# Performance work log

Measured on AMD Instinct MI355X. Metric: run time of the kernel, lower is better.

Reference implementation:

```python
import jax, jax.numpy as jnp
import numpy as np

B, L, H, O = 2048, 256, 512, 1  # batch, input_len, hidden_size, output_size
EPS = 1e-5

def setup_inputs() -> dict:
    key = jax.random.key(0)
    ks = jax.random.split(key, 16)
    s = 0.05
    return {
        "x": jax.random.normal(ks[0], (B, 1, O), jnp.float32),
        "hidden": jax.random.normal(ks[1], (1, B, H), jnp.float32),
        "encoder_outputs": jax.random.normal(ks[2], (B, L, H), jnp.float32),
        # weights stored [in, out] (transposed torch Linear convention)
        "emb_W": jax.random.normal(ks[3], (O, H), jnp.float32) * s,
        "emb_b": jax.random.normal(ks[4], (H,), jnp.float32) * s,
        "attn_W": jax.random.normal(ks[5], (2 * H, L), jnp.float32) * s,
        "attn_b": jax.random.normal(ks[6], (L,), jnp.float32) * s,
        "comb_W": jax.random.normal(ks[7], (2 * H, H), jnp.float32) * s,
        "comb_b": jax.random.normal(ks[8], (H,), jnp.float32) * s,
        "gru_Wih": jax.random.normal(ks[9], (H, 3 * H), jnp.float32) * s,
        "gru_Whh": jax.random.normal(ks[10], (H, 3 * H), jnp.float32) * s,
        "gru_bih": jax.random.normal(ks[11], (3 * H,), jnp.float32) * s,
        "gru_bhh": jax.random.normal(ks[12], (3 * H,), jnp.float32) * s,
        "out_W": jax.random.normal(ks[13], (H, O), jnp.float32) * s,
        "out_b": jax.random.normal(ks[14], (O,), jnp.float32) * s,
    }

def reference(x, hidden, encoder_outputs, emb_W, emb_b, attn_W, attn_b,
              comb_W, comb_b, gru_Wih, gru_Whh, gru_bih, gru_bhh, out_W, out_b):
    # embedding + InstanceNorm1d over hidden dim (C=1 channel, length=H), no affine
    embedded = x @ emb_W + emb_b                      # [B,1,H]
    mu = jnp.mean(embedded, axis=-1, keepdims=True)
    var = jnp.var(embedded, axis=-1, keepdims=True)   # biased var, matches torch
    embedded = (embedded - mu) * jax.lax.rsqrt(var + EPS)
    # dropout = identity (inference)
    h_b = jnp.transpose(hidden, (1, 0, 2))            # [B,1,H]
    attn_logits = jnp.concatenate([embedded, h_b], axis=2) @ attn_W + attn_b  # [B,1,L]
    attn_weights = jax.nn.softmax(attn_logits, axis=2)
    attn_applied = jnp.einsum('bql,bld->bqd', attn_weights, encoder_outputs)  # [B,1,H]
    out = jnp.concatenate([embedded, attn_applied], axis=2) @ comb_W + comb_b
    out = jax.nn.relu(out)                            # [B,1,H]
    # single GRU step (num_layers=1, seq_len=1)
    xt = out[:, 0, :]                                 # [B,H]
    h0 = hidden[0]                                    # [B,H]
    gi = xt @ gru_Wih + gru_bih                       # [B,3H]
    gh = h0 @ gru_Whh + gru_bhh
    i_r, i_z, i_n = jnp.split(gi, 3, axis=-1)
    h_r, h_z, h_n = jnp.split(gh, 3, axis=-1)
    r = jax.nn.sigmoid(i_r + h_r)
    z = jax.nn.sigmoid(i_z + h_z)
    n = jnp.tanh(i_n + r * h_n)
    h_new = (1.0 - z) * n + z * h0                    # [B,H]
    output = h_new[:, None, :] @ out_W + out_b        # [B,1,O]
    return output, h_new[None, :, :], attn_weights
```

## Files before the change

### kernel.cpp

```cpp
#include <hip/hip_runtime.h>
#include <math.h>

#define NB 2048
#define NL 256
#define NH 512

typedef unsigned short ushort_t;
typedef short s16x8 __attribute__((ext_vector_type(8)));
typedef short s16x4 __attribute__((ext_vector_type(4)));
typedef float f32x4 __attribute__((ext_vector_type(4)));

__device__ __forceinline__ float wsum(float v){
  #pragma unroll
  for (int o = 32; o; o >>= 1) v += __shfl_xor(v, o);
  return v;
}
__device__ __forceinline__ float wmax(float v){
  #pragma unroll
  for (int o = 32; o; o >>= 1) v = fmaxf(v, __shfl_xor(v, o));
  return v;
}
__device__ __forceinline__ ushort_t f2bf(float f){
  union { float f; unsigned u; } v; v.f = f;
  unsigned r = v.u + 0x7fffu + ((v.u >> 16) & 1u);
  return (ushort_t)(r >> 16);
}

__global__ __launch_bounds__(256)
void kPrepAll(const float* __restrict__ hidden,
              const float* __restrict__ eW, const float* __restrict__ eb,
              const float* __restrict__ attn_W, const float* __restrict__ comb_W,
              const float* __restrict__ Wih, const float* __restrict__ Whh,
              const float* __restrict__ out_b,
              ushort_t* __restrict__ A2, ushort_t* __restrict__ WTG,
              ushort_t* __restrict__ WTA, ushort_t* __restrict__ WTC,
              float* __restrict__ stats,
              float* __restrict__ p, float* __restrict__ q,
              float* __restrict__ p2, float* __restrict__ q2,
              float* __restrict__ out0)
{
  const int bid = blockIdx.x, tid = threadIdx.x;
  if (bid < 512) {
    const int idx = (bid*256 + tid) * 8;
    const int b = idx >> 9, h = idx & 511;
    float4 v0 = *(const float4*)(hidden + idx);
    float4 v1 = *(const float4*)(hidden + idx + 4);
    s16x8 o;
    o[0]=f2bf(v0.x); o[1]=f2bf(v0.y); o[2]=f2bf(v0.z); o[3]=f2bf(v0.w);
    o[4]=f2bf(v1.x); o[5]=f2bf(v1.y); o[6]=f2bf(v1.z); o[7]=f2bf(v1.w);
    *(s16x8*)&A2[(size_t)b*1024 + 512 + h] = o;
    return;
  }
  if (bid < 1024) {
    const int b2 = bid - 512, bx = b2 & 31, by = b2 >> 5;
    const int n = bx*64 + (tid & 63);
    const int ksub = by*64 + (tid >> 6)*16;
    const int g = n >> 6, t = (n >> 4) & 3, c = (g << 4) | (n & 15);
    const int sc = (t == 0) ? c : (t == 1) ? (512 + c) : (1024 + c);
    ushort_t vals[16];
    #pragma unroll
    for (int kk = 0; kk < 16; ++kk) {
      int k = ksub + kk;
      float v;
      if (k < 512) v = (t == 3) ? 0.f : Wih[(size_t)k*1536 + sc];
      else         v = (t == 2) ? 0.f : Whh[(size_t)(k-512)*1536 + sc];
      vals[kk] = f2bf(v);
    }
    *(s16x8*)&WTG[(size_t)n*1024 + ksub]     = *(s16x8*)&vals[0];
    *(s16x8*)&WTG[(size_t)n*1024 + ksub + 8] = *(s16x8*)&vals[8];
    return;
  }
  if (bid < 1056) {
    const int b2 = bid - 1024, bx = b2 & 3, by = b2 >> 2;
    const int c = bx*64 + (tid & 63);
    const int ksub = by*64 + (tid >> 6)*16;
    ushort_t vals[16];
    #pragma unroll
    for (int kk = 0; kk < 16; ++kk)
      vals[kk] = f2bf(attn_W[(size_t)(512 + ksub + kk)*NL + c]);
    *(s16x8*)&WTA[(size_t)c*512 + ksub]     = *(s16x8*)&vals[0];
    *(s16x8*)&WTA[(size_t)c*512 + ksub + 8] = *(s16x8*)&vals[8];
    return;
  }
  if (bid < 1120) {
    const int b2 = bid - 1056, bx = b2 & 7, by = b2 >> 3;
    const int c = bx*64 + (tid & 63);
    const int ksub = by*64 + (tid >> 6)*16;
    ushort_t vals[16];
    #pragma unroll
    for (int kk = 0; kk < 16; ++kk)
      vals[kk] = f2bf(comb_W[(size_t)(512 + ksub + kk)*NH + c]);
    *(s16x8*)&WTC[(size_t)c*512 + ksub]     = *(s16x8*)&vals[0];
    *(s16x8*)&WTC[(size_t)c*512 + ksub + 8] = *(s16x8*)&vals[8];
    return;
  }
  if (bid > 1132) {
    out0[(bid-1133)*256 + tid] = out_b[0];
    return;
  }
  {
    __shared__ float rw[4], rb[4];
    __shared__ float pa[4][64], pb[4][64];
    const int lane = tid & 63, wv = tid >> 6;
    float swv = eW[tid] + eW[tid + 256];
    float sbv = eb[tid] + eb[tid + 256];
    swv = wsum(swv); sbv = wsum(sbv);
    if (lane == 0) { rw[wv] = swv; rb[wv] = sbv; }
    __syncthreads();
    const float mW = (rw[0]+rw[1]+rw[2]+rw[3]) * (1.f/NH);
    const float mb = (rb[0]+rb[1]+rb[2]+rb[3]) * (1.f/NH);

    if (bid == 1132) {
      float u0 = eW[tid]-mW, u1 = eW[tid+256]-mW;
      float v0 = eb[tid]-mb, v1 = eb[tid+256]-mb;
      float s2 = u0*u0 + u1*u1, s3 = u0*v0 + u1*v1, s4 = v0*v0 + v1*v1;
      s2 = wsum(s2); s3 = wsum(s3); s4 = wsum(s4);
      if (lane == 0) { pa[0][wv] = s2; pa[1][wv] = s3; pa[2][wv] = s4; }
      __syncthreads();
      if (tid == 0) {
        stats[0] = mW; stats[1] = mb;
        stats[2] = pa[0][0]+pa[0][1]+pa[0][2]+pa[0][3];
        stats[3] = pa[1][0]+pa[1][1]+pa[1][2]+pa[1][3];
        stats[4] = pa[2][0]+pa[2][1]+pa[2][2]+pa[2][3];
      }
      return;
    }
    const int bid2 = bid - 1120;
    const float* Wsrc; int ldw, c0; float *op, *oq;
    if (bid2 < 4) { Wsrc = attn_W; ldw = NL; c0 = bid2*64;     op = p  + c0; oq = q  + c0; }
    else          { Wsrc = comb_W; ldw = NH; c0 = (bid2-4)*64; op = p2 + c0; oq = q2 + c0; }
    const int c = c0 + lane;
    const int hc = tid >> 6;
    float ap = 0.f, aq = 0.f;
    #pragma unroll 4
    for (int h = hc*128; h < hc*128 + 128; ++h) {
      float w = Wsrc[(size_t)h*ldw + c];
      ap = fmaf(eW[h]-mW, w, ap);
      aq = fmaf(eb[h]-mb, w, aq);
    }
    pa[hc][lane] = ap; pb[hc][lane] = aq;
    __syncthreads();
    if (hc == 0) {
      op[lane] = pa[0][lane]+pa[1][lane]+pa[2][lane]+pa[3][lane];
      oq[lane] = pb[0][lane]+pb[1][lane]+pb[2][lane]+pb[3][lane];
    }
  }
}

template<int EPI>
__global__ __launch_bounds__(256)
void gemm_bf16(const ushort_t* __restrict__ A, int lda,
               const ushort_t* __restrict__ Bt, int K,
               const float* __restrict__ xin, const float* __restrict__ stats,
               const float* __restrict__ pvec, const float* __restrict__ qvec,
               const float* __restrict__ bias,
               float* __restrict__ out_f, ushort_t* __restrict__ out_bf,
               const float* __restrict__ bih, const float* __restrict__ bhh,
               const float* __restrict__ hidden, const float* __restrict__ out_W,
               float* __restrict__ h_out, float* __restrict__ out0)
{
  __shared__ ushort_t As[128][72];
  __shared__ ushort_t Bs[64][72];
  const int tid = threadIdx.x, lane = tid & 63, wr = tid >> 6;
  const int m0 = blockIdx.x * 128, n0 = blockIdx.y * 64;

  f32x4 acc[2][4];
  #pragma unroll
  for (int i = 0; i < 2; ++i)
    #pragma unroll
    for (int j = 0; j < 4; ++j)
      acc[i][j] = (f32x4){0.f,0.f,0.f,0.f};

  const int srow = tid >> 3, scol = (tid & 7) * 8;
  for (int kt = 0; kt < K; kt += 64) {
    __syncthreads();
    #pragma unroll
    for (int it = 0; it < 4; ++it) {
      const int r = srow + it*32;
      *(s16x8*)&As[r][scol] = *(const s16x8*)&A[(size_t)(m0+r)*lda + kt + scol];
    }
    #pragma unroll
    for (int it = 0; it < 2; ++it) {
      const int r = srow + it*32;
      *(s16x8*)&Bs[r][scol] = *(const s16x8*)&Bt[(size_t)(n0+r)*K + kt + scol];
    }
    __syncthreads();
    #pragma unroll
    for (int ks = 0; ks < 2; ++ks) {
      const int ko = ks*32 + (lane >> 4)*8;
      s16x8 af[2], bfr[4];
      #pragma unroll
      for (int i = 0; i < 2; ++i) af[i]  = *(const s16x8*)&As[wr*32 + i*16 + (lane & 15)][ko];
      #pragma unroll
      for (int j = 0; j < 4; ++j) bfr[j] = *(const s16x8*)&Bs[j*16 + (lane & 15)][ko];
      #pragma unroll
      for (int i = 0; i < 2; ++i)
        #pragma unroll
        for (int j = 0; j < 4; ++j)
          acc[i][j] = __builtin_amdgcn_mfma_f32_16x16x32_bf16(af[i], bfr[j], acc[i][j], 0, 0, 0);
    }
  }

  if constexpr (EPI == 1 || EPI == 2) {
    const float S2 = stats[2], S3 = stats[3], S4 = stats[4];
    #pragma unroll
    for (int i = 0; i < 2; ++i) {
      #pragma unroll
      for (int reg = 0; reg < 4; ++reg) {
        const int row = m0 + wr*32 + i*16 + ((lane >> 4) << 2) + reg;
        const float xv = xin[row];
        const float rs = rsqrtf((xv*xv*S2 + 2.f*xv*S3 + S4)*(1.0f/NH) + 1e-5f);
        const float al = xv*rs, be = rs;
        #pragma unroll
        for (int j = 0; j < 4; ++j) {
          const int col = n0 + j*16 + (lane & 15);
          float v = acc[i][j][reg] + bias[col] + al*pvec[col] + be*qvec[col];
          if constexpr (EPI == 1) out_f[(size_t)row*NL + col] = v;
          else                    out_bf[(size_t)row*1024 + col] = f2bf(fmaxf(v, 0.f));
        }
      }
    }
  } else {
    const int g = n0 >> 6;
    const int hcol = (g << 4) | (lane & 15);
    const float b_r = bih[hcol]        + bhh[hcol];
    const float b_z = bih[512 + hcol]  + bhh[512 + hcol];
    const float b_i = bih[1024 + hcol];
    const float b_h = bhh[1024 + hcol];
    const float ow  = out_W[hcol];
    #pragma unroll
    for (int i = 0; i < 2; ++i) {
      #pragma unroll
      for (int reg = 0; reg < 4; ++reg) {
        const int row = m0 + wr*32 + i*16 + ((lane >> 4) << 2) + reg;
        float rv = 1.f / (1.f + expf(-(acc[i][0][reg] + b_r)));
        float zv = 1.f / (1.f + expf(-(acc[i][1][reg] + b_z)));
        float nv = tanhf(acc[i][2][reg] + b_i + rv * (acc[i][3][reg] + b_h));
        float h0v = hidden[(size_t)row*NH + hcol];
        float hn = nv + zv * (h0v - nv);
        h_out[(size_t)row*NH + hcol] = hn;
        float partial = hn * ow;
        #pragma unroll
        for (int o = 1; o < 16; o <<= 1) partial += __shfl_xor(partial, o);
        if ((lane & 15) == 0) atomicAdd(&out0[row], partial);
      }
    }
  }
}

__global__ __launch_bounds__(256)
void kStream(const float* __restrict__ logits, const float* __restrict__ enc,
             float* __restrict__ attn_out, ushort_t* __restrict__ ABF)
{
  __shared__ float wl[NL];
  __shared__ __align__(16) float4 ps[128];
  __shared__ float sred[4];
  const int tid = threadIdx.x, lane = tid & 63, wv = tid >> 6;
  const int b = blockIdx.x;

  float lg = logits[(size_t)b*NL + tid];
  float m = wmax(lg);
  if (lane == 0) sred[wv] = m;
  __syncthreads();
  m = fmaxf(fmaxf(sred[0], sred[1]), fmaxf(sred[2], sred[3]));
  float e = expf(lg - m);
  float s = wsum(e);
  __syncthreads();
  if (lane == 0) sred[wv] = s;
  __syncthreads();
  const float inv = 1.f / (sred[0] + sred[1] + sred[2] + sred[3]);
  e *= inv;
  wl[tid] = e;
  attn_out[(size_t)b*NL + tid] = e;
  __syncthreads();

  const int col = tid & 127, half = tid >> 7;
  const float4* ep = (const float4*)(enc + (size_t)b*NL*NH);
  float4 acc = {0.f,0.f,0.f,0.f};
  #pragma unroll 4
  for (int l = half*128; l < half*128 + 128; ++l) {
    float w = wl[l];
    float4 ev = ep[l*(NH/4) + col];
    acc.x = fmaf(w,ev.x,acc.x); acc.y = fmaf(w,ev.y,acc.y);
    acc.z = fmaf(w,ev.z,acc.z); acc.w = fmaf(w,ev.w,acc.w);
  }
  if (half == 0) ps[col] = acc;
  __syncthreads();
  if (half == 1) {
    float4 o = ps[col];
    o.x += acc.x; o.y += acc.y; o.z += acc.z; o.w += acc.w;
    s16x4 ov; ov[0]=f2bf(o.x); ov[1]=f2bf(o.y); ov[2]=f2bf(o.z); ov[3]=f2bf(o.w);
    *(s16x4*)&ABF[(size_t)b*NH + col*4] = ov;
  }
}

extern "C" void kernel_launch(void* const* d_in, const int* in_sizes, int n_in,
                              void* d_out, int out_size, void* d_ws, size_t ws_size,
                              hipStream_t stream)
{
  const float* x      = (const float*)d_in[0];
  const float* hidden = (const float*)d_in[1];
  const float* enc    = (const float*)d_in[2];
  const float* emb_W  = (const float*)d_in[3];
  const float* emb_b  = (const float*)d_in[4];
  const float* attn_W = (const float*)d_in[5];
  const float* attn_b = (const float*)d_in[6];
  const float* comb_W = (const float*)d_in[7];
  const float* comb_b = (const float*)d_in[8];
  const float* Wih    = (const float*)d_in[9];
  const float* Whh    = (const float*)d_in[10];
  const float* bih    = (const float*)d_in[11];
  const float* bhh    = (const float*)d_in[12];
  const float* out_W  = (const float*)d_in[13];
  const float* out_b  = (const float*)d_in[14];

  float* out      = (float*)d_out;
  float* out0     = out;
  float* out_h    = out + NB;
  float* out_attn = out + NB + (size_t)NB*NH;

  float* wsf    = (float*)d_ws;
  float* stats  = wsf;
  float* p      = wsf + 16;
  float* q      = wsf + 272;
  float* p2     = wsf + 528;
  float* q2     = wsf + 1040;
  float* logits = wsf + 2048;
  ushort_t* usb = (ushort_t*)(wsf + 526400);
  ushort_t* A2  = usb;
  ushort_t* ABF = usb + 2097152;
  ushort_t* WTA = usb + 3145728;
  ushort_t* WTC = usb + 3276800;
  ushort_t* WTG = usb + 3538944;

  kPrepAll<<<1141, 256, 0, stream>>>(hidden, emb_W, emb_b, attn_W, comb_W,
                                     Wih, Whh, out_b, A2, WTG, WTA, WTC,
                                     stats, p, q, p2, q2, out0);
  gemm_bf16<1><<<dim3(16, 4), 256, 0, stream>>>(A2 + 512, 1024, WTA, 512,
      x, stats, p, q, attn_b, logits, nullptr,
      nullptr, nullptr, nullptr, nullptr, nullptr, nullptr);
  kStream<<<NB, 256, 0, stream>>>(logits, enc, out_attn, ABF);
  gemm_bf16<2><<<dim3(16, 8), 256, 0, stream>>>(ABF, 512, WTC, 512,
      x, stats, p2, q2, comb_b, nullptr, A2,
      nullptr, nullptr, nullptr, nullptr, nullptr, nullptr);
  gemm_bf16<3><<<dim3(16, 32), 256, 0, stream>>>(A2, 1024, WTG, 1024,
      nullptr, nullptr, nullptr, nullptr, nullptr, nullptr, nullptr,
      bih, bhh, hidden, out_W, out_h, out0);
}
```

Measured before the change: 265.7 us.

## Move weight conversion into stream kernel, load fp32 hidden directly, enlarge GRU tiles

The prep kernel is split. Only the small attention-weight transpose and the statistics stay ahead of the logits GEMM. The hidden-state bf16 conversion and the GRU and comb weight transposes move into the memory-bound attention stream kernel as extra blocks, so they can overlap with the encoder streaming. The logits GEMM now converts fp32 hidden to bf16 itself while staging it, which takes the large prep kernel off the critical path. The GRU GEMM switches to 128x128 tiles with a 2x2 wave layout, so each block does more work on B-tile reuse, at the cost of fewer blocks and more registers.

```diff
diff --git a/kernel.cpp b/kernel.cpp
--- a/kernel.cpp
+++ b/kernel.cpp
@@ -6,6 +6,7 @@
 #define NH 512
 
 typedef unsigned short ushort_t;
+typedef unsigned int uint_t;
 typedef short s16x8 __attribute__((ext_vector_type(8)));
 typedef short s16x4 __attribute__((ext_vector_type(4)));
 typedef float f32x4 __attribute__((ext_vector_type(4)));
@@ -27,51 +28,17 @@
 }
 
 __global__ __launch_bounds__(256)
-void kPrepAll(const float* __restrict__ hidden,
-              const float* __restrict__ eW, const float* __restrict__ eb,
-              const float* __restrict__ attn_W, const float* __restrict__ comb_W,
-              const float* __restrict__ Wih, const float* __restrict__ Whh,
-              const float* __restrict__ out_b,
-              ushort_t* __restrict__ A2, ushort_t* __restrict__ WTG,
-              ushort_t* __restrict__ WTA, ushort_t* __restrict__ WTC,
-              float* __restrict__ stats,
-              float* __restrict__ p, float* __restrict__ q,
-              float* __restrict__ p2, float* __restrict__ q2,
-              float* __restrict__ out0)
+void kTiny(const float* __restrict__ eW, const float* __restrict__ eb,
+           const float* __restrict__ attn_W, const float* __restrict__ comb_W,
+           const float* __restrict__ out_b,
+           ushort_t* __restrict__ WTA, float* __restrict__ stats,
+           float* __restrict__ p, float* __restrict__ q,
+           float* __restrict__ p2, float* __restrict__ q2,
+           float* __restrict__ out0)
 {
   const int bid = blockIdx.x, tid = threadIdx.x;
-  if (bid < 512) {
-    const int idx = (bid*256 + tid) * 8;
-    const int b = idx >> 9, h = idx & 511;
-    float4 v0 = *(const float4*)(hidden + idx);
-    float4 v1 = *(const float4*)(hidden + idx + 4);
-    s16x8 o;
-    o[0]=f2bf(v0.x); o[1]=f2bf(v0.y); o[2]=f2bf(v0.z); o[3]=f2bf(v0.w);
-    o[4]=f2bf(v1.x); o[5]=f2bf(v1.y); o[6]=f2bf(v1.z); o[7]=f2bf(v1.w);
-    *(s16x8*)&A2[(size_t)b*1024 + 512 + h] = o;
-    return;
-  }
-  if (bid < 1024) {
-    const int b2 = bid - 512, bx = b2 & 31, by = b2 >> 5;
-    const int n = bx*64 + (tid & 63);
-    const int ksub = by*64 + (tid >> 6)*16;
-    const int g = n >> 6, t = (n >> 4) & 3, c = (g << 4) | (n & 15);
-    const int sc = (t == 0) ? c : (t == 1) ? (512 + c) : (1024 + c);
-    ushort_t vals[16];
-    #pragma unroll
-    for (int kk = 0; kk < 16; ++kk) {
-      int k = ksub + kk;
-      float v;
-      if (k < 512) v = (t == 3) ? 0.f : Wih[(size_t)k*1536 + sc];
-      else         v = (t == 2) ? 0.f : Whh[(size_t)(k-512)*1536 + sc];
-      vals[kk] = f2bf(v);
-    }
-    *(s16x8*)&WTG[(size_t)n*1024 + ksub]     = *(s16x8*)&vals[0];
-    *(s16x8*)&WTG[(size_t)n*1024 + ksub + 8] = *(s16x8*)&vals[8];
-    return;
-  }
-  if (bid < 1056) {
-    const int b2 = bid - 1024, bx = b2 & 3, by = b2 >> 2;
+  if (bid < 32) {
+    const int bx = bid & 3, by = bid >> 2;
     const int c = bx*64 + (tid & 63);
     const int ksub = by*64 + (tid >> 6)*16;
     ushort_t vals[16];
@@ -82,20 +49,8 @@
     *(s16x8*)&WTA[(size_t)c*512 + ksub + 8] = *(s16x8*)&vals[8];
     return;
   }
-  if (bid < 1120) {
-    const int b2 = bid - 1056, bx = b2 & 7, by = b2 >> 3;
-    const int c = bx*64 + (tid & 63);
-    const int ksub = by*64 + (tid >> 6)*16;
-    ushort_t vals[16];
-    #pragma unroll
-    for (int kk = 0; kk < 16; ++kk)
-      vals[kk] = f2bf(comb_W[(size_t)(512 + ksub + kk)*NH + c]);
-    *(s16x8*)&WTC[(size_t)c*512 + ksub]     = *(s16x8*)&vals[0];
-    *(s16x8*)&WTC[(size_t)c*512 + ksub + 8] = *(s16x8*)&vals[8];
-    return;
-  }
-  if (bid > 1132) {
-    out0[(bid-1133)*256 + tid] = out_b[0];
+  if (bid > 44) {
+    out0[(bid-45)*256 + tid] = out_b[0];
     return;
   }
   {
@@ -110,7 +65,7 @@
     const float mW = (rw[0]+rw[1]+rw[2]+rw[3]) * (1.f/NH);
     const float mb = (rb[0]+rb[1]+rb[2]+rb[3]) * (1.f/NH);
 
-    if (bid == 1132) {
+    if (bid == 44) {
       float u0 = eW[tid]-mW, u1 = eW[tid+256]-mW;
       float v0 = eb[tid]-mb, v1 = eb[tid+256]-mb;
       float s2 = u0*u0 + u1*u1, s3 = u0*v0 + u1*v1, s4 = v0*v0 + v1*v1;
@@ -125,7 +80,7 @@
       }
       return;
     }
-    const int bid2 = bid - 1120;
+    const int bid2 = bid - 32;
     const float* Wsrc; int ldw, c0; float *op, *oq;
     if (bid2 < 4) { Wsrc = attn_W; ldw = NL; c0 = bid2*64;     op = p  + c0; oq = q  + c0; }
     else          { Wsrc = comb_W; ldw = NH; c0 = (bid2-4)*64; op = p2 + c0; oq = q2 + c0; }
@@ -147,17 +102,11 @@
   }
 }
 
-template<int EPI>
 __global__ __launch_bounds__(256)
-void gemm_bf16(const ushort_t* __restrict__ A, int lda,
-               const ushort_t* __restrict__ Bt, int K,
-               const float* __restrict__ xin, const float* __restrict__ stats,
-               const float* __restrict__ pvec, const float* __restrict__ qvec,
-               const float* __restrict__ bias,
-               float* __restrict__ out_f, ushort_t* __restrict__ out_bf,
-               const float* __restrict__ bih, const float* __restrict__ bhh,
-               const float* __restrict__ hidden, const float* __restrict__ out_W,
-               float* __restrict__ h_out, float* __restrict__ out0)
+void kLogits(const float* __restrict__ hidden, const ushort_t* __restrict__ WTA,
+             const float* __restrict__ x, const float* __restrict__ stats,
+             const float* __restrict__ p, const float* __restrict__ q,
+             const float* __restrict__ attn_b, float* __restrict__ logits)
 {
   __shared__ ushort_t As[128][72];
   __shared__ ushort_t Bs[64][72];
@@ -172,17 +121,23 @@
       acc[i][j] = (f32x4){0.f,0.f,0.f,0.f};
 
   const int srow = tid >> 3, scol = (tid & 7) * 8;
-  for (int kt = 0; kt < K; kt += 64) {
+  for (int kt = 0; kt < 512; kt += 64) {
     __syncthreads();
     #pragma unroll
     for (int it = 0; it < 4; ++it) {
       const int r = srow + it*32;
-      *(s16x8*)&As[r][scol] = *(const s16x8*)&A[(size_t)(m0+r)*lda + kt + scol];
+      const float* hp = hidden + (size_t)(m0+r)*NH + kt + scol;
+      float4 v0 = *(const float4*)hp;
+      float4 v1 = *(const float4*)(hp + 4);
+      s16x8 o;
+      o[0]=f2bf(v0.x); o[1]=f2bf(v0.y); o[2]=f2bf(v0.z); o[3]=f2bf(v0.w);
+      o[4]=f2bf(v1.x); o[5]=f2bf(v1.y); o[6]=f2bf(v1.z); o[7]=f2bf(v1.w);
+      *(s16x8*)&As[r][scol] = o;
     }
     #pragma unroll
     for (int it = 0; it < 2; ++it) {
       const int r = srow + it*32;
-      *(s16x8*)&Bs[r][scol] = *(const s16x8*)&Bt[(size_t)(n0+r)*K + kt + scol];
+      *(s16x8*)&Bs[r][scol] = *(const s16x8*)&WTA[(size_t)(n0+r)*512 + kt + scol];
     }
     __syncthreads();
     #pragma unroll
@@ -201,96 +156,256 @@
     }
   }
 
-  if constexpr (EPI == 1 || EPI == 2) {
-    const float S2 = stats[2], S3 = stats[3], S4 = stats[4];
-    #pragma unroll
-    for (int i = 0; i < 2; ++i) {
-      #pragma unroll
-      for (int reg = 0; reg < 4; ++reg) {
-        const int row = m0 + wr*32 + i*16 + ((lane >> 4) << 2) + reg;
-        const float xv = xin[row];
-        const float rs = rsqrtf((xv*xv*S2 + 2.f*xv*S3 + S4)*(1.0f/NH) + 1e-5f);
-        const float al = xv*rs, be = rs;
+  const float S2 = stats[2], S3 = stats[3], S4 = stats[4];
+  #pragma unroll
+  for (int i = 0; i < 2; ++i) {
+    #pragma unroll
+    for (int reg = 0; reg < 4; ++reg) {
+      const int row = m0 + wr*32 + i*16 + ((lane >> 4) << 2) + reg;
+      const float xv = x[row];
+      const float rs = rsqrtf((xv*xv*S2 + 2.f*xv*S3 + S4)*(1.0f/NH) + 1e-5f);
+      const float al = xv*rs, be = rs;
+      #pragma unroll
+      for (int j = 0; j < 4; ++j) {
+        const int col = n0 + j*16 + (lane & 15);
+        logits[(size_t)row*NL + col] = acc[i][j][reg] + attn_b[col] + al*p[col] + be*q[col];
+      }
+    }
+  }
+}
+
+__global__ __launch_bounds__(256)
+void kStreamMega(const float* __restrict__ hidden,
+                 const float* __restrict__ Wih, const float* __restrict__ Whh,
+                 const float* __restrict__ comb_W,
+                 const float* __restrict__ logits, const float* __restrict__ enc,
+                 ushort_t* __restrict__ A2, ushort_t* __restrict__ WTG,
+                 ushort_t* __restrict__ WTC,
+                 float* __restrict__ attn_out, ushort_t* __restrict__ ABF)
+{
+  const int bid = blockIdx.x, tid = threadIdx.x;
+  if (bid < 512) {
+    const int idx = (bid*256 + tid) * 8;
+    const int b = idx >> 9, h = idx & 511;
+    float4 v0 = *(const float4*)(hidden + idx);
+    float4 v1 = *(const float4*)(hidden + idx + 4);
+    s16x8 o;
+    o[0]=f2bf(v0.x); o[1]=f2bf(v0.y); o[2]=f2bf(v0.z); o[3]=f2bf(v0.w);
+    o[4]=f2bf(v1.x); o[5]=f2bf(v1.y); o[6]=f2bf(v1.z); o[7]=f2bf(v1.w);
+    *(s16x8*)&A2[(size_t)b*1024 + 512 + h] = o;
+    return;
+  }
+  if (bid < 1024) {
+    const int b2 = bid - 512, bx = b2 & 31, by = b2 >> 5;
+    const int n = bx*64 + (tid & 63);
+    const int ksub = by*64 + (tid >> 6)*16;
+    const int g = n >> 6, t = (n >> 4) & 3, c = (g << 4) | (n & 15);
+    const int sc = (t == 0) ? c : (t == 1) ? (512 + c) : (1024 + c);
+    ushort_t vals[16];
+    #pragma unroll
+    for (int kk = 0; kk < 16; ++kk) {
+      int k = ksub + kk;
+      float v;
+      if (k < 512) v = (t == 3) ? 0.f : Wih[(size_t)k*1536 + sc];
+      else         v = (t == 2) ? 0.f : Whh[(size_t)(k-512)*1536 + sc];
+      vals[kk] = f2bf(v);
+    }
+    *(s16x8*)&WTG[(size_t)n*1024 + ksub]     = *(s16x8*)&vals[0];
+    *(s16x8*)&WTG[(size_t)n*1024 + ksub + 8] = *(s16x8*)&vals[8];
+    return;
+  }
+  if (bid < 1088) {
+    const int b2 = bid - 1024, bx = b2 & 7, by = b2 >> 3;
+    const int c = bx*64 + (tid & 63);
+    const int ksub = by*64 + (tid >> 6)*16;
+    ushort_t vals[16];
+    #pragma unroll
+    for (int kk = 0; kk < 16; ++kk)
+      vals[kk] = f2bf(comb_W[(size_t)(512 + ksub + kk)*NH + c]);
+    *(s16x8*)&WTC[(size_t)c*512 + ksub]     = *(s16x8*)&vals[0];
+    *(s16x8*)&WTC[(size_t)c*512 + ksub + 8] = *(s16x8*)&vals[8];
+    return;
+  }
+  {
+    __shared__ float wl[NL];
+    __shared__ __align__(16) float4 ps[128];
+    __shared__ float sred[4];
+    const int lane = tid & 63, wv = tid >> 6;
+    const int b = bid - 1088;
+
+    float lg = logits[(size_t)b*NL + tid];
+    float m = wmax(lg);
+    if (lane == 0) sred[wv] = m;
+    __syncthreads();
+    m = fmaxf(fmaxf(sred[0], sred[1]), fmaxf(sred[2], sred[3]));
+    float e = expf(lg - m);
+    float s = wsum(e);
+    __syncthreads();
+    if (lane == 0) sred[wv] = s;
+    __syncthreads();
+    const float inv = 1.f / (sred[0] + sred[1] + sred[2] + sred[3]);
+    e *= inv;
+    wl[tid] = e;
+    attn_out[(size_t)b*NL + tid] = e;
+    __syncthreads();
+
+    const int col = tid & 127, half = tid >> 7;
+    const float4* ep = (const float4*)(enc + (size_t)b*NL*NH);
+    float4 acc = {0.f,0.f,0.f,0.f};
+    #pragma unroll 4
+    for (int l = half*128; l < half*128 + 128; ++l) {
+      float w = wl[l];
+      float4 ev = ep[l*(NH/4) + col];
+      acc.x = fmaf(w,ev.x,acc.x); acc.y = fmaf(w,ev.y,acc.y);
+      acc.z = fmaf(w,ev.z,acc.z); acc.w = fmaf(w,ev.w,acc.w);
+    }
+    if (half == 0) ps[col] = acc;
+    __syncthreads();
+    if (half == 1) {
+      float4 o = ps[col];
+      o.x += acc.x; o.y += acc.y; o.z += acc.z; o.w += acc.w;
+      s16x4 ov; ov[0]=f2bf(o.x); ov[1]=f2bf(o.y); ov[2]=f2bf(o.z); ov[3]=f2bf(o.w);
+      *(s16x4*)&ABF[(size_t)b*NH + col*4] = ov;
+    }
+  }
+}
+
+__global__ __launch_bounds__(256)
+void kComb(const ushort_t* __restrict__ ABF, const ushort_t* __restrict__ WTC,
+           const float* __restrict__ x, const float* __restrict__ stats,
+           const float* __restrict__ p2, const float* __restrict__ q2,
+           const float* __restrict__ comb_b, ushort_t* __restrict__ A2)
+{
+  __shared__ ushort_t As[128][72];
+  __shared__ ushort_t Bs[64][72];
+  const int tid = threadIdx.x, lane = tid & 63, wr = tid >> 6;
+  const int m0 = blockIdx.x * 128, n0 = blockIdx.y * 64;
+
+  f32x4 acc[2][4];
+  #pragma unroll
+  for (int i = 0; i < 2; ++i)
+    #pragma unroll
+    for (int j = 0; j < 4; ++j)
+      acc[i][j] = (f32x4){0.f,0.f,0.f,0.f};
+
+  const int srow = tid >> 3, scol = (tid & 7) * 8;
+  for (int kt = 0; kt < 512; kt += 64) {
+    __syncthreads();
+    #pragma unroll
+    for (int it = 0; it < 4; ++it) {
+      const int r = srow + it*32;
+      *(s16x8*)&As[r][scol] = *(const s16x8*)&ABF[(size_t)(m0+r)*512 + kt + scol];
+    }
+    #pragma unroll
+    for (int it = 0; it < 2; ++it) {
+      const int r = srow + it*32;
+      *(s16x8*)&Bs[r][scol] = *(const s16x8*)&WTC[(size_t)(n0+r)*512 + kt + scol];
+    }
+    __syncthreads();
+    #pragma unroll
+    for (int ks = 0; ks < 2; ++ks) {
+      const int ko = ks*32 + (lane >> 4)*8;
+      s16x8 af[2], bfr[4];
+      #pragma unroll
+      for (int i = 0; i < 2; ++i) af[i]  = *(const s16x8*)&As[wr*32 + i*16 + (lane & 15)][ko];
+      #pragma unroll
+      for (int j = 0; j < 4; ++j) bfr[j] = *(const s16x8*)&Bs[j*16 + (lane & 15)][ko];
+      #pragma unroll
+      for (int i = 0; i < 2; ++i)
         #pragma unroll
-        for (int j = 0; j < 4; ++j) {
-          const int col = n0 + j*16 + (lane & 15);
-          float v = acc[i][j][reg] + bias[col] + al*pvec[col] + be*qvec[col];
-          if constexpr (EPI == 1) out_f[(size_t)row*NL + col] = v;
-          else                    out_bf[(size_t)row*1024 + col] = f2bf(fmaxf(v, 0.f));
-        }
+        for (int j = 0; j < 4; ++j)
+          acc[i][j] = __builtin_amdgcn_mfma_f32_16x16x32_bf16(af[i], bfr[j], acc[i][j], 0, 0, 0);
+    }
+  }
+
+  const float S2 = stats[2], S3 = stats[3], S4 = stats[4];
+  #pragma unroll
+  for (int i = 0; i < 2; ++i) {
+    #pragma unroll
+    for (int reg = 0; reg < 4; ++reg) {
+      const int row = m0 + wr*32 + i*16 + ((lane >> 4) << 2) + reg;
+      const float xv = x[row];
+      const float rs = rsqrtf((xv*xv*S2 + 2.f*xv*S3 + S4)*(1.0f/NH) + 1e-5f);
+      const float al = xv*rs, be = rs;
+      #pragma unroll
+      for (int j = 0; j < 4; ++j) {
+        const int col = n0 + j*16 + (lane & 15);
+        float v = acc[i][j][reg] + comb_b[col] + al*p2[col] + be*q2[col];
+        A2[(size_t)row*1024 + col] = f2bf(fmaxf(v, 0.f));
       }
     }
-  } else {
-    const int g = n0 >> 6;
-    const int hcol = (g << 4) | (lane & 15);
-    const float b_r = bih[hcol]        + bhh[hcol];
-    const float b_z = bih[512 + hcol]  + bhh[512 + hcol];
-    const float b_i = bih[1024 + hcol];
-    const float b_h = bhh[1024 + hcol];
-    const float ow  = out_W[hcol];
-    #pragma unroll
-    for (int i = 0; i < 2; ++i) {
-      #pragma unroll
-      for (int reg = 0; reg < 4; ++reg) {
-        const int row = m0 + wr*32 + i*16 + ((lane >> 4) << 2) + reg;
-        float rv = 1.f / (1.f + expf(-(acc[i][0][reg] + b_r)));
-        float zv = 1.f / (1.f + expf(-(acc[i][1][reg] + b_z)));
-        float nv = tanhf(acc[i][2][reg] + b_i + rv * (acc[i][3][reg] + b_h));
-        float h0v = hidden[(size_t)row*NH + hcol];
-        float hn = nv + zv * (h0v - nv);
-        h_out[(size_t)row*NH + hcol] = hn;
-        float partial = hn * ow;
+  }
+}
+
+__global__ __launch_bounds__(256)
+void kGRU(const ushort_t* __restrict__ A, const ushort_t* __restrict__ Bt,
+          const float* __restrict__ bih, const float* __restrict__ bhh,
+          const float* __restrict__ hidden, const float* __restrict__ out_W,
+          float* __restrict__ h_out, float* __restrict__ out0)
+{
+  __shared__ ushort_t As[128][72];
+  __shared__ ushort_t Bs[128][72];
+  const int tid = threadIdx.x, lane = tid & 63, wv = tid >> 6;
+  const int wr = wv >> 1, wc = wv & 1;
+  const int m0 = blockIdx.x * 128, n0 = blockIdx.y * 128;
+
+  f32x4 acc[4][4];
+  #pragma unroll
+  for (int i = 0; i < 4; ++i)
+    #pragma unroll
+    for (int j = 0; j < 4; ++j)
+      acc[i][j] = (f32x4){0.f,0.f,0.f,0.f};
+
+  const int srow = tid >> 3, scol = (tid & 7) * 8;
+  for (int kt = 0; kt < 1024; kt += 64) {
+    __syncthreads();
+    #pragma unroll
+    for (int it = 0; it < 4; ++it) {
+      const int r = srow + it*32;
+      *(s16x8*)&As[r][scol] = *(const s16x8*)&A [(size_t)(m0+r)*1024 + kt + scol];
+      *(s16x8*)&Bs[r][scol] = *(const s16x8*)&Bt[(size_t)(n0+r)*1024 + kt + scol];
+    }
+    __syncthreads();
+    #pragma unroll
+    for (int ks = 0; ks < 2; ++ks) {
+      const int ko = ks*32 + (lane >> 4)*8;
+      s16x8 af[4], bfr[4];
+      #pragma unroll
+      for (int f = 0; f < 4; ++f) {
+        af[f]  = *(const s16x8*)&As[wr*64 + f*16 + (lane & 15)][ko];
+        bfr[f] = *(const s16x8*)&Bs[wc*64 + f*16 + (lane & 15)][ko];
+      }
+      #pragma unroll
+      for (int i = 0; i < 4; ++i)
         #pragma unroll
-        for (int o = 1; o < 16; o <<= 1) partial += __shfl_xor(partial, o);
-        if ((lane & 15) == 0) atomicAdd(&out0[row], partial);
-      }
-    }
-  }
-}
-
-__global__ __launch_bounds__(256)
-void kStream(const float* __restrict__ logits, const float* __restrict__ enc,
-             float* __restrict__ attn_out, ushort_t* __restrict__ ABF)
-{
-  __shared__ float wl[NL];
-  __shared__ __align__(16) float4 ps[128];
-  __shared__ float sred[4];
-  const int tid = threadIdx.x, lane = tid & 63, wv = tid >> 6;
-  const int b = blockIdx.x;
-
-  float lg = logits[(size_t)b*NL + tid];
-  float m = wmax(lg);
-  if (lane == 0) sred[wv] = m;
-  __syncthreads();
-  m = fmaxf(fmaxf(sred[0], sred[1]), fmaxf(sred[2], sred[3]));
-  float e = expf(lg - m);
-  float s = wsum(e);
-  __syncthreads();
-  if (lane == 0) sred[wv] = s;
-  __syncthreads();
-  const float inv = 1.f / (sred[0] + sred[1] + sred[2] + sred[3]);
-  e *= inv;
-  wl[tid] = e;
-  attn_out[(size_t)b*NL + tid] = e;
-  __syncthreads();
-
-  const int col = tid & 127, half = tid >> 7;
-  const float4* ep = (const float4*)(enc + (size_t)b*NL*NH);
-  float4 acc = {0.f,0.f,0.f,0.f};
-  #pragma unroll 4
-  for (int l = half*128; l < half*128 + 128; ++l) {
-    float w = wl[l];
-    float4 ev = ep[l*(NH/4) + col];
-    acc.x = fmaf(w,ev.x,acc.x); acc.y = fmaf(w,ev.y,acc.y);
-    acc.z = fmaf(w,ev.z,acc.z); acc.w = fmaf(w,ev.w,acc.w);
-  }
-  if (half == 0) ps[col] = acc;
-  __syncthreads();
-  if (half == 1) {
-    float4 o = ps[col];
-    o.x += acc.x; o.y += acc.y; o.z += acc.z; o.w += acc.w;
-    s16x4 ov; ov[0]=f2bf(o.x); ov[1]=f2bf(o.y); ov[2]=f2bf(o.z); ov[3]=f2bf(o.w);
-    *(s16x4*)&ABF[(size_t)b*NH + col*4] = ov;
+        for (int j = 0; j < 4; ++j)
+          acc[i][j] = __builtin_amdgcn_mfma_f32_16x16x32_bf16(af[i], bfr[j], acc[i][j], 0, 0, 0);
+    }
+  }
+
+  const int g = (n0 >> 6) + wc;
+  const int hcol = (g << 4) | (lane & 15);
+  const float b_r = bih[hcol]        + bhh[hcol];
+  const float b_z = bih[512 + hcol]  + bhh[512 + hcol];
+  const float b_i = bih[1024 + hcol];
+  const float b_h = bhh[1024 + hcol];
+  const float ow  = out_W[hcol];
+  #pragma unroll
+  for (int i = 0; i < 4; ++i) {
+    #pragma unroll
+    for (int reg = 0; reg < 4; ++reg) {
+      const int row = m0 + wr*64 + i*16 + ((lane >> 4) << 2) + reg;
+      float rv = 1.f / (1.f + expf(-(acc[i][0][reg] + b_r)));
+      float zv = 1.f / (1.f + expf(-(acc[i][1][reg] + b_z)));
+      float nv = tanhf(acc[i][2][reg] + b_i + rv * (acc[i][3][reg] + b_h));
+      float h0v = hidden[(size_t)row*NH + hcol];
+      float hn = nv + zv * (h0v - nv);
+      h_out[(size_t)row*NH + hcol] = hn;
+      float partial = hn * ow;
+      #pragma unroll
+      for (int o = 1; o < 16; o <<= 1) partial += __shfl_xor(partial, o);
+      if ((lane & 15) == 0) atomicAdd(&out0[row], partial);
+    }
   }
 }
 
@@ -333,17 +448,13 @@
   ushort_t* WTC = usb + 3276800;
   ushort_t* WTG = usb + 3538944;
 
-  kPrepAll<<<1141, 256, 0, stream>>>(hidden, emb_W, emb_b, attn_W, comb_W,
-                                     Wih, Whh, out_b, A2, WTG, WTA, WTC,
-                                     stats, p, q, p2, q2, out0);
-  gemm_bf16<1><<<dim3(16, 4), 256, 0, stream>>>(A2 + 512, 1024, WTA, 512,
-      x, stats, p, q, attn_b, logits, nullptr,
-      nullptr, nullptr, nullptr, nullptr, nullptr, nullptr);
-  kStream<<<NB, 256, 0, stream>>>(logits, enc, out_attn, ABF);
-  gemm_bf16<2><<<dim3(16, 8), 256, 0, stream>>>(ABF, 512, WTC, 512,
-      x, stats, p2, q2, comb_b, nullptr, A2,
-      nullptr, nullptr, nullptr, nullptr, nullptr, nullptr);
-  gemm_bf16<3><<<dim3(16, 32), 256, 0, stream>>>(A2, 1024, WTG, 1024,
-      nullptr, nullptr, nullptr, nullptr, nullptr, nullptr, nullptr,
-      bih, bhh, hidden, out_W, out_h, out0);
-}
+  kTiny<<<53, 256, 0, stream>>>(emb_W, emb_b, attn_W, comb_W, out_b,
+                                WTA, stats, p, q, p2, q2, out0);
+  kLogits<<<dim3(16, 4), 256, 0, stream>>>(hidden, WTA, x, stats, p, q,
+                                           attn_b, logits);
+  kStreamMega<<<3136, 256, 0, stream>>>(hidden, Wih, Whh, comb_W, logits, enc,
+                                        A2, WTG, WTC, out_attn, ABF);
+  kComb<<<dim3(16, 8), 256, 0, stream>>>(ABF, WTC, x, stats, p2, q2, comb_b, A2);
+  kGRU<<<dim3(16, 16), 256, 0, stream>>>(A2, WTG, bih, bhh, hidden, out_W,
+                                         out_h, out0);
+}
```

Measured after the change: 281.1 us. +5.8%, slower.
